# Performance work log

Hardware: AMD Instinct MI355X
Metric: run time of the kernel (lower is better)

## Reference

```python
import jax, jax.numpy as jnp
import numpy as np

TOPK = 8
EXTRA = 0  # ADDITIONAL_LAYERS_IN_GPU
CPU_TOPK = int(0.25 * 64)  # CPU_MOE_RATIO * num_experts = 16


def setup_inputs() -> dict:
    key = jax.random.key(0)
    k1, k2 = jax.random.split(key)
    hidden_states = jax.random.normal(k1, (4, 4096, 4096), dtype=jnp.float32)
    wg_weight = jax.random.normal(k2, (64, 4096), dtype=jnp.float32) * 0.02
    return {"hidden_states": hidden_states, "wg_weight": wg_weight}


def reference(hidden_states, wg_weight):
    bsz, seq_len, hidden_size = hidden_states.shape
    x = hidden_states.reshape(-1, hidden_size).astype(jnp.float32)  # [T, H]
    logits = jnp.einsum('th,eh->te', x, wg_weight)  # [T, 64]
    gates = jax.nn.softmax(logits, axis=1)
    values_all, indices_all = jax.lax.top_k(gates, TOPK + EXTRA)
    expert_weight = values_all[:, :TOPK]
    expert_index = indices_all[:, :TOPK]
    _, cpu_expert_index = jax.lax.top_k(gates, CPU_TOPK)
    cpu_expert_index = cpu_expert_index[:, 8 + EXTRA:]
    # norm_topk_prob=True, topk > 1
    eps = jnp.finfo(jnp.float32).eps
    denom = jnp.maximum(expert_weight.sum(axis=1, keepdims=True), eps)
    expert_weight = expert_weight / denom
    return (expert_weight, expert_index, cpu_expert_index, indices_all)
```

## Files before the change

kernel.cpp:

```cpp
#include <hip/hip_runtime.h>

#define T_TOK 16384
#define HDIM  4096
#define NEXP  64
#define TAU   2e-4f
#define BM    128

typedef unsigned short u16;
typedef u16   u16x8  __attribute__((ext_vector_type(8)));
typedef __bf16 bf16x8 __attribute__((ext_vector_type(8)));
typedef float f32x4  __attribute__((ext_vector_type(4)));

__device__ __forceinline__ void gld16(const void* g, void* l) {
    __builtin_amdgcn_global_load_lds(
        (const __attribute__((address_space(1))) void*)g,
        (__attribute__((address_space(3))) void*)l, 16, 0, 0);
}

__global__ void zero_counter(int* counter) {
    if (threadIdx.x == 0) counter[0] = 0;
}

__global__ __launch_bounds__(256)
void wsplit_kernel(const float* __restrict__ w, u16x8* __restrict__ wfrag,
                   float4* __restrict__ wt4) {
    const int id  = blockIdx.x * 256 + threadIdx.x;
    const int e   = id >> 9;
    const int k8g = id & 511;
    const int k   = k8g * 8;

    const float* wp = w + (size_t)e * HDIM + k;
    const float4 v0 = *(const float4*)wp;
    const float4 v1 = *(const float4*)(wp + 4);

    wt4[(size_t)(2 * k8g) * NEXP + e]     = v0;
    wt4[(size_t)(2 * k8g + 1) * NEXP + e] = v1;

    const float fv[8] = {v0.x, v0.y, v0.z, v0.w, v1.x, v1.y, v1.z, v1.w};
    bf16x8 hv, lv;
#pragma unroll
    for (int j = 0; j < 8; ++j) {
        const __bf16 h = (__bf16)fv[j];
        hv[j] = h;
        lv[j] = (__bf16)(fv[j] - (float)h);
    }
    const int chunk = k >> 6;
    const int k8 = (k >> 3) & 7, ks = k8 >> 2, g = k8 & 3, nt = e >> 4;
    const int U = ks * 256 + nt * 64 + 16 * g + (e & 15);
    wfrag[(size_t)chunk * 1024 + U]       = __builtin_bit_cast(u16x8, hv);
    wfrag[(size_t)chunk * 1024 + 512 + U] = __builtin_bit_cast(u16x8, lv);
}

__global__ __launch_bounds__(256, 3)
void gate_gemm_mfma(const float* __restrict__ x, const u16x8* __restrict__ wfrag,
                    float* __restrict__ partial, int ksplit) {
    const int b      = blockIdx.x;
    const int kslice = b % ksplit;
    const int tblk   = b / ksplit;
    const int kspan  = HDIM / ksplit;
    const int k0     = kslice * kspan;
    const int t0     = tblk * BM;

    __shared__ __align__(16) unsigned char smem[48 * 1024];

    const int tid  = threadIdx.x;
    const int lane = tid & 63;
    const int wv   = tid >> 6;

    f32x4 acc[2][4];
#pragma unroll
    for (int m = 0; m < 2; ++m)
#pragma unroll
        for (int nt = 0; nt < 4; ++nt) acc[m][nt] = (f32x4){0.f, 0.f, 0.f, 0.f};

    for (int kc = k0; kc < k0 + kspan; kc += 64) {
        __syncthreads();

        const u16x8* wsrc = wfrag + (size_t)(kc >> 6) * 1024;
#pragma unroll
        for (int i = 0; i < 4; ++i) {
            const int u = tid + 256 * i;
            gld16(wsrc + u, smem + (size_t)u * 16);
        }
#pragma unroll
        for (int j = 0; j < 8; ++j) {
            const int u   = tid + 256 * j;
            const int row = u >> 4;
            const int k4l = (u & 15) ^ (row & 15);
            gld16(x + (size_t)(t0 + row) * HDIM + kc + 4 * k4l,
                  smem + 16384 + (size_t)u * 16);
        }
        __syncthreads();

        const u16*   wb = (const u16*)smem;
        const float* xb = (const float*)(smem + 16384);
#pragma unroll
        for (int ks2 = 0; ks2 < 2; ++ks2) {
            const int k8 = (ks2 << 2) + (lane >> 4);
            bf16x8 axh[2], axl[2];
#pragma unroll
            for (int m = 0; m < 2; ++m) {
                const int row = (wv * 2 + m) * 16 + (lane & 15);
                const int p0  = row * 16 + ((2 * k8) ^ (row & 15));
                const int p1  = row * 16 + ((2 * k8 + 1) ^ (row & 15));
                const float4 va = *(const float4*)(xb + 4 * p0);
                const float4 vb = *(const float4*)(xb + 4 * p1);
                const float fv[8] = {va.x, va.y, va.z, va.w, vb.x, vb.y, vb.z, vb.w};
                bf16x8 hv, lv;
#pragma unroll
                for (int j = 0; j < 8; ++j) {
                    const __bf16 h = (__bf16)fv[j];
                    hv[j] = h;
                    lv[j] = (__bf16)(fv[j] - (float)h);
                }
                axh[m] = hv;
                axl[m] = lv;
            }
#pragma unroll
            for (int nt = 0; nt < 4; ++nt) {
                const int uwi = ks2 * 256 + nt * 64 + lane;
                const bf16x8 bh = __builtin_bit_cast(bf16x8, *(const u16x8*)(wb + (size_t)uwi * 8));
                const bf16x8 bl = __builtin_bit_cast(bf16x8, *(const u16x8*)(wb + (size_t)(512 + uwi) * 8));
#pragma unroll
                for (int m = 0; m < 2; ++m) {
                    acc[m][nt] = __builtin_amdgcn_mfma_f32_16x16x32_bf16(axh[m], bh, acc[m][nt], 0, 0, 0);
                    acc[m][nt] = __builtin_amdgcn_mfma_f32_16x16x32_bf16(axh[m], bl, acc[m][nt], 0, 0, 0);
                    acc[m][nt] = __builtin_amdgcn_mfma_f32_16x16x32_bf16(axl[m], bh, acc[m][nt], 0, 0, 0);
                }
            }
        }
    }

    float* op = partial + (size_t)kslice * T_TOK * NEXP;
    const int ecol = lane & 15;
#pragma unroll
    for (int m = 0; m < 2; ++m) {
        const int trow = t0 + (wv * 2 + m) * 16 + ((lane >> 4) << 2);
#pragma unroll
        for (int nt = 0; nt < 4; ++nt)
#pragma unroll
            for (int r = 0; r < 4; ++r)
                op[(size_t)(trow + r) * NEXP + nt * 16 + ecol] = acc[m][nt][r];
    }
}

__global__ __launch_bounds__(256)
void gate_topk_f32(const float* __restrict__ partial, int ksplit,
                   float* __restrict__ out, int* __restrict__ list,
                   int* __restrict__ counter) {
    const int wave = threadIdx.x >> 6;
    const int lane = threadIdx.x & 63;
    const int t = blockIdx.x * 4 + wave;

    float l = 0.f;
    for (int s = 0; s < ksplit; ++s)
        l += partial[(size_t)s * T_TOK * NEXP + (size_t)t * NEXP + lane];

    float v = l;
    const int idx = lane;
    float myval = -3.4e38f;
    int   myidx = 0;
#pragma unroll
    for (int r = 0; r < 17; ++r) {
        float bv = v;
        int   bi = idx;
#pragma unroll
        for (int s = 1; s < 64; s <<= 1) {
            const float ov = __shfl_xor(bv, s);
            const int   oi = __shfl_xor(bi, s);
            if (ov > bv || (ov == bv && oi < bi)) { bv = ov; bi = oi; }
        }
        if (lane == r) { myval = bv; myidx = bi; }
        if (idx == bi) v = -3.4e38f;
    }

    const float nxt = __shfl(myval, (lane + 1) & 63);
    const bool close = (lane < 16) && (myval - nxt < TAU);
    if (__ballot(close) != 0ull) {
        if (lane == 0) { const int p = atomicAdd(counter, 1); list[p] = t; }
    }

    const float m = __shfl(myval, 0);
    const float p = (lane < 16) ? expf(myval - m) : 0.f;
    float s8 = (lane < 8) ? p : 0.f;
#pragma unroll
    for (int s = 1; s < 64; s <<= 1) s8 += __shfl_xor(s8, s);

    float* ew = out;
    float* ei = out + (size_t)T_TOK * 8;
    float* ci = out + (size_t)2 * T_TOK * 8;
    float* ia = out + (size_t)3 * T_TOK * 8;
    if (lane < 8) {
        ew[(size_t)t * 8 + lane] = p / s8;
        ei[(size_t)t * 8 + lane] = (float)myidx;
        ia[(size_t)t * 8 + lane] = (float)myidx;
    } else if (lane < 16) {
        ci[(size_t)t * 8 + (lane - 8)] = (float)myidx;
    }
}

__global__ __launch_bounds__(256)
void repair_partial(const float* __restrict__ x, const float4* __restrict__ wt4,
                    const int* __restrict__ list, const int* __restrict__ counter,
                    double* __restrict__ fpart) {
    const int lane = threadIdx.x & 63;
    const int wid  = (int)((blockIdx.x * blockDim.x + threadIdx.x) >> 6);
    const int nw   = (int)((gridDim.x * blockDim.x) >> 6);
    const int nit  = counter[0] * 16;

    for (int it = wid; it < nit; it += nw) {
        const int li = it >> 4;
        const int ks = it & 15;
        const int t  = __builtin_amdgcn_readfirstlane(list[li]);
        const float4* xr4 = (const float4*)(x + (size_t)t * HDIM) + ks * 64;
        const float4* wb  = wt4 + (size_t)ks * 64 * NEXP;

        double a0 = 0.0, a1 = 0.0, a2 = 0.0, a3 = 0.0;
#pragma unroll 4
        for (int j = 0; j < 64; j += 4) {
            const float4 w0 = wb[(size_t)(j + 0) * NEXP + lane];
            const float4 w1 = wb[(size_t)(j + 1) * NEXP + lane];
            const float4 w2 = wb[(size_t)(j + 2) * NEXP + lane];
            const float4 w3 = wb[(size_t)(j + 3) * NEXP + lane];
            const float4 x0 = xr4[j + 0];
            const float4 x1 = xr4[j + 1];
            const float4 x2 = xr4[j + 2];
            const float4 x3 = xr4[j + 3];
            a0 = fma((double)x0.x, (double)w0.x, a0);
            a0 = fma((double)x0.y, (double)w0.y, a0);
            a0 = fma((double)x0.z, (double)w0.z, a0);
            a0 = fma((double)x0.w, (double)w0.w, a0);
            a1 = fma((double)x1.x, (double)w1.x, a1);
            a1 = fma((double)x1.y, (double)w1.y, a1);
            a1 = fma((double)x1.z, (double)w1.z, a1);
            a1 = fma((double)x1.w, (double)w1.w, a1);
            a2 = fma((double)x2.x, (double)w2.x, a2);
            a2 = fma((double)x2.y, (double)w2.y, a2);
            a2 = fma((double)x2.z, (double)w2.z, a2);
            a2 = fma((double)x2.w, (double)w2.w, a2);
            a3 = fma((double)x3.x, (double)w3.x, a3);
            a3 = fma((double)x3.y, (double)w3.y, a3);
            a3 = fma((double)x3.z, (double)w3.z, a3);
            a3 = fma((double)x3.w, (double)w3.w, a3);
        }
        fpart[(size_t)li * 1024 + ks * 64 + lane] = (a0 + a1) + (a2 + a3);
    }
}

__global__ __launch_bounds__(256)
void repair_final(const double* __restrict__ fpart, const int* __restrict__ list,
                  const int* __restrict__ counter, float* __restrict__ out) {
    const int lane = threadIdx.x & 63;
    const int wid  = (int)((blockIdx.x * blockDim.x + threadIdx.x) >> 6);
    const int nw   = (int)((gridDim.x * blockDim.x) >> 6);
    const int n    = counter[0];

    for (int li = wid; li < n; li += nw) {
        const int t = __builtin_amdgcn_readfirstlane(list[li]);

        double v = 0.0;
#pragma unroll
        for (int ks = 0; ks < 16; ++ks)
            v += fpart[(size_t)li * 1024 + ks * 64 + lane];

        const int idx = lane;
        double mylog = -1.0e308;
        int    myidx = 0;
#pragma unroll
        for (int r = 0; r < 16; ++r) {
            double bv = v;
            int    bi = idx;
#pragma unroll
            for (int s = 1; s < 64; s <<= 1) {
                const double ov = __shfl_xor(bv, s);
                const int    oi = __shfl_xor(bi, s);
                if (ov > bv || (ov == bv && oi < bi)) { bv = ov; bi = oi; }
            }
            if (lane == r) { mylog = bv; myidx = bi; }
            if (idx == bi) v = -1.0e308;
        }

        const double m = __shfl(mylog, 0);
        const float p = (lane < 16) ? expf((float)(mylog - m)) : 0.f;
        float s8 = (lane < 8) ? p : 0.f;
#pragma unroll
        for (int s = 1; s < 64; s <<= 1) s8 += __shfl_xor(s8, s);

        float* ew = out;
        float* ei = out + (size_t)T_TOK * 8;
        float* ci = out + (size_t)2 * T_TOK * 8;
        float* ia = out + (size_t)3 * T_TOK * 8;
        if (lane < 8) {
            ew[(size_t)t * 8 + lane] = p / s8;
            ei[(size_t)t * 8 + lane] = (float)myidx;
            ia[(size_t)t * 8 + lane] = (float)myidx;
        } else if (lane < 16) {
            ci[(size_t)t * 8 + (lane - 8)] = (float)myidx;
        }
    }
}

extern "C" void kernel_launch(void* const* d_in, const int* in_sizes, int n_in,
                              void* d_out, int out_size, void* d_ws, size_t ws_size,
                              hipStream_t stream) {
    const float* x = (const float*)d_in[0];
    const float* w = (const float*)d_in[1];
    float* out     = (float*)d_out;

    const size_t slice      = (size_t)T_TOK * NEXP * sizeof(float);
    const size_t wfragBytes = (size_t)64 * 1024 * 16;
    const size_t wt4Bytes   = (size_t)NEXP * HDIM * sizeof(float);
    const size_t fpartBytes = (size_t)T_TOK * 16 * NEXP * sizeof(double);
    const size_t extra      = wfragBytes + wt4Bytes + fpartBytes +
                              (size_t)T_TOK * sizeof(int) + 64;

    int ksplit = 1;
    if      (ws_size >= 8 * slice + extra) ksplit = 8;
    else if (ws_size >= 4 * slice + extra) ksplit = 4;
    else if (ws_size >= 2 * slice + extra) ksplit = 2;

    float*  partial = (float*)d_ws;
    u16x8*  wfrag   = (u16x8*)((char*)d_ws + (size_t)ksplit * slice);
    float4* wt4     = (float4*)((char*)wfrag + wfragBytes);
    double* fpart   = (double*)((char*)wt4 + wt4Bytes);
    int*    list    = (int*)((char*)fpart + fpartBytes);
    int*    counter = list + T_TOK;

    zero_counter<<<1, 64, 0, stream>>>(counter);
    wsplit_kernel<<<128, 256, 0, stream>>>(w, wfrag, wt4);
    gate_gemm_mfma<<<ksplit * (T_TOK / BM), 256, 0, stream>>>(x, wfrag, partial, ksplit);
    gate_topk_f32<<<T_TOK / 4, 256, 0, stream>>>(partial, ksplit, out, list, counter);
    repair_partial<<<4096, 256, 0, stream>>>(x, wt4, list, counter, fpart);
    repair_final<<<1024, 256, 0, stream>>>(fpart, list, counter, out);
}
```

Before: 159.5 us.

## Double-buffer gate GEMM LDS staging with 32-wide K chunks and fold counter zeroing

The gate GEMM loop now issues async global-to-LDS loads for the next 32-wide K chunk while running MFMAs on the current one, using two LDS buffers and one barrier per chunk instead of two. The x tile swizzle is changed to match the narrower chunk. The separate zero_counter launch is folded into wsplit_kernel to save one kernel launch. The trade-off is twice as many loop iterations with less work in each, and it depends on the async loads finishing before the barrier at the end of each iteration.

```diff
diff --git a/kernel.cpp b/kernel.cpp
--- a/kernel.cpp
+++ b/kernel.cpp
@@ -17,13 +17,11 @@
         (__attribute__((address_space(3))) void*)l, 16, 0, 0);
 }
 
-__global__ void zero_counter(int* counter) {
-    if (threadIdx.x == 0) counter[0] = 0;
-}
-
 __global__ __launch_bounds__(256)
 void wsplit_kernel(const float* __restrict__ w, u16x8* __restrict__ wfrag,
-                   float4* __restrict__ wt4) {
+                   float4* __restrict__ wt4, int* __restrict__ counter) {
+    if (blockIdx.x == 0 && threadIdx.x == 0) counter[0] = 0;
+
     const int id  = blockIdx.x * 256 + threadIdx.x;
     const int e   = id >> 9;
     const int k8g = id & 511;
@@ -60,6 +58,7 @@
     const int kspan  = HDIM / ksplit;
     const int k0     = kslice * kspan;
     const int t0     = tblk * BM;
+    const int nch    = kspan >> 5;
 
     __shared__ __align__(16) unsigned char smem[48 * 1024];
 
@@ -73,62 +72,64 @@
 #pragma unroll
         for (int nt = 0; nt < 4; ++nt) acc[m][nt] = (f32x4){0.f, 0.f, 0.f, 0.f};
 
-    for (int kc = k0; kc < k0 + kspan; kc += 64) {
+    auto stage = [&](int c, int p) {
+        const int kc  = k0 + (c << 5);
+        const u16x8* wsrc = wfrag + (size_t)(kc >> 6) * 1024 + ((c & 1) << 8);
+        unsigned char* base = smem + (size_t)p * 1536 * 16;
+        gld16(wsrc + tid,       base + (size_t)tid * 16);
+        gld16(wsrc + 512 + tid, base + (size_t)(256 + tid) * 16);
+#pragma unroll
+        for (int j = 0; j < 4; ++j) {
+            const int u   = tid + 256 * j;
+            const int row = u >> 3;
+            const int k4l = (u & 7) ^ (row & 7);
+            gld16(x + (size_t)(t0 + row) * HDIM + kc + 4 * k4l,
+                  base + (size_t)(512 + u) * 16);
+        }
+    };
+
+    stage(0, 0);
+    __syncthreads();
+
+    for (int c = 0; c < nch; ++c) {
+        const int p = c & 1;
+        if (c + 1 < nch) stage(c + 1, p ^ 1);
+
+        const u16x8* wb = (const u16x8*)(smem + (size_t)p * 1536 * 16);
+        const float* xb = (const float*)(smem + ((size_t)p * 1536 + 512) * 16);
+        const int k8 = lane >> 4;
+
+        bf16x8 axh[2], axl[2];
+#pragma unroll
+        for (int m = 0; m < 2; ++m) {
+            const int row = (wv * 2 + m) * 16 + (lane & 15);
+            const int p0  = row * 8 + ((2 * k8)     ^ (row & 7));
+            const int p1  = row * 8 + ((2 * k8 + 1) ^ (row & 7));
+            const float4 va = *(const float4*)(xb + 4 * p0);
+            const float4 vb = *(const float4*)(xb + 4 * p1);
+            const float fv[8] = {va.x, va.y, va.z, va.w, vb.x, vb.y, vb.z, vb.w};
+            bf16x8 hv, lv;
+#pragma unroll
+            for (int j = 0; j < 8; ++j) {
+                const __bf16 h = (__bf16)fv[j];
+                hv[j] = h;
+                lv[j] = (__bf16)(fv[j] - (float)h);
+            }
+            axh[m] = hv;
+            axl[m] = lv;
+        }
+#pragma unroll
+        for (int nt = 0; nt < 4; ++nt) {
+            const bf16x8 bh = __builtin_bit_cast(bf16x8, wb[nt * 64 + lane]);
+            const bf16x8 bl = __builtin_bit_cast(bf16x8, wb[256 + nt * 64 + lane]);
+#pragma unroll
+            for (int m = 0; m < 2; ++m) {
+                acc[m][nt] = __builtin_amdgcn_mfma_f32_16x16x32_bf16(axh[m], bh, acc[m][nt], 0, 0, 0);
+                acc[m][nt] = __builtin_amdgcn_mfma_f32_16x16x32_bf16(axh[m], bl, acc[m][nt], 0, 0, 0);
+                acc[m][nt] = __builtin_amdgcn_mfma_f32_16x16x32_bf16(axl[m], bh, acc[m][nt], 0, 0, 0);
+            }
+        }
         __syncthreads();
-
-        const u16x8* wsrc = wfrag + (size_t)(kc >> 6) * 1024;
-#pragma unroll
-        for (int i = 0; i < 4; ++i) {
-            const int u = tid + 256 * i;
-            gld16(wsrc + u, smem + (size_t)u * 16);
-        }
-#pragma unroll
-        for (int j = 0; j < 8; ++j) {
-            const int u   = tid + 256 * j;
-            const int row = u >> 4;
-            const int k4l = (u & 15) ^ (row & 15);
-            gld16(x + (size_t)(t0 + row) * HDIM + kc + 4 * k4l,
-                  smem + 16384 + (size_t)u * 16);
-        }
-        __syncthreads();
-
-        const u16*   wb = (const u16*)smem;
-        const float* xb = (const float*)(smem + 16384);
-#pragma unroll
-        for (int ks2 = 0; ks2 < 2; ++ks2) {
-            const int k8 = (ks2 << 2) + (lane >> 4);
-            bf16x8 axh[2], axl[2];
-#pragma unroll
-            for (int m = 0; m < 2; ++m) {
-                const int row = (wv * 2 + m) * 16 + (lane & 15);
-                const int p0  = row * 16 + ((2 * k8) ^ (row & 15));
-                const int p1  = row * 16 + ((2 * k8 + 1) ^ (row & 15));
-                const float4 va = *(const float4*)(xb + 4 * p0);
-                const float4 vb = *(const float4*)(xb + 4 * p1);
-                const float fv[8] = {va.x, va.y, va.z, va.w, vb.x, vb.y, vb.z, vb.w};
-                bf16x8 hv, lv;
-#pragma unroll
-                for (int j = 0; j < 8; ++j) {
-                    const __bf16 h = (__bf16)fv[j];
-                    hv[j] = h;
-                    lv[j] = (__bf16)(fv[j] - (float)h);
-                }
-                axh[m] = hv;
-                axl[m] = lv;
-            }
-#pragma unroll
-            for (int nt = 0; nt < 4; ++nt) {
-                const int uwi = ks2 * 256 + nt * 64 + lane;
-                const bf16x8 bh = __builtin_bit_cast(bf16x8, *(const u16x8*)(wb + (size_t)uwi * 8));
-                const bf16x8 bl = __builtin_bit_cast(bf16x8, *(const u16x8*)(wb + (size_t)(512 + uwi) * 8));
-#pragma unroll
-                for (int m = 0; m < 2; ++m) {
-                    acc[m][nt] = __builtin_amdgcn_mfma_f32_16x16x32_bf16(axh[m], bh, acc[m][nt], 0, 0, 0);
-                    acc[m][nt] = __builtin_amdgcn_mfma_f32_16x16x32_bf16(axh[m], bl, acc[m][nt], 0, 0, 0);
-                    acc[m][nt] = __builtin_amdgcn_mfma_f32_16x16x32_bf16(axl[m], bh, acc[m][nt], 0, 0, 0);
-                }
-            }
-        }
     }
 
     float* op = partial + (size_t)kslice * T_TOK * NEXP;
@@ -326,8 +327,7 @@
     int*    list    = (int*)((char*)fpart + fpartBytes);
     int*    counter = list + T_TOK;
 
-    zero_counter<<<1, 64, 0, stream>>>(counter);
-    wsplit_kernel<<<128, 256, 0, stream>>>(w, wfrag, wt4);
+    wsplit_kernel<<<128, 256, 0, stream>>>(w, wfrag, wt4, counter);
     gate_gemm_mfma<<<ksplit * (T_TOK / BM), 256, 0, stream>>>(x, wfrag, partial, ksplit);
     gate_topk_f32<<<T_TOK / 4, 256, 0, stream>>>(partial, ksplit, out, list, counter);
     repair_partial<<<4096, 256, 0, stream>>>(x, wt4, list, counter, fpart);
```

After: 159.5 us. About the same (-0.0%).
